# Kernel optimization log

Measured on AMD Instinct MI355X. Metric: run time of the kernel, lower is better.

The kernel has to match this reference:

```python
import jax, jax.numpy as jnp
import numpy as np

NUM_EMBEDDINGS = 512
EMBEDDING_DIM = 64
SPARSITY_LEVEL = 5
COMMITMENT_COST = 0.25
EPSILON = 1e-10


def setup_inputs() -> dict:
    key = jax.random.key(0)
    k1, k2 = jax.random.split(key)
    z_e = jax.random.normal(k1, (32, EMBEDDING_DIM, 32, 32), dtype=jnp.float32)
    D = jax.random.normal(k2, (EMBEDDING_DIM, NUM_EMBEDDINGS), dtype=jnp.float32)
    # module normalizes atoms at init (normalize_atoms=True)
    D = D / (jnp.linalg.norm(D, axis=0, keepdims=True) + 1e-10)
    return {"z_e": z_e, "dictionary": D}


def batch_omp(X, D, sparsity, eps):
    """Greedy batched OMP. X: [M, B] signals, D: [M, N] unit-norm atoms -> coeffs [N, B]."""
    M, B = X.shape
    N = D.shape[1]
    bidx = jnp.arange(B)

    def step(carry, _):
        coeffs, residual, mask = carry
        corr = D.T @ residual                      # [N, B]
        idx = jnp.argmax(jnp.abs(corr) * mask, axis=0)  # [B]
        mask = mask.at[idx, bidx].set(0.0)
        d_sel = D[:, idx]                          # [M, B] gather of selected atoms
        alpha = jnp.sum(residual * d_sel, axis=0) / (jnp.sum(d_sel * d_sel, axis=0) + eps)
        coeffs = coeffs.at[idx, bidx].set(alpha)   # scatter coefficient
        residual = residual - d_sel * alpha[None, :]
        return (coeffs, residual, mask), None

    init = (jnp.zeros((N, B), X.dtype), X, jnp.ones((N, B), X.dtype))
    (coeffs, _, _), _ = jax.lax.scan(step, init, None, length=sparsity)
    return coeffs


def reference(z_e, dictionary):
    B, C, H, W = z_e.shape
    L = H * W
    # patch_size=1: unfold -> [B, C, L]; permute(2,0,1) -> [L, B, C]; flatten -> [L*B, C]; .T -> [C, L*B]
    tokens = z_e.reshape(B, C, L).transpose(2, 0, 1).reshape(L * B, C).T
    xf = tokens.astype(jnp.float32)
    Df = dictionary.astype(jnp.float32)
    atom_norms = jnp.maximum(jnp.linalg.norm(Df, axis=0), 1e-10)
    Dn = Df / atom_norms[None, :]                  # normalized dictionary (used for OMP and recon)
    coefficients = batch_omp(xf, Dn, SPARSITY_LEVEL, EPSILON)  # [N, L*B]
    z_dl_f32 = Dn @ coefficients                   # [C, L*B]
    # fold back: [L*B, C] -> [L, B, C] -> [B, C, L] -> [B, C, H, W]
    z_dl = z_dl_f32.T.reshape(L, B, C).transpose(1, 2, 0).reshape(B, C, H, W).astype(z_e.dtype)
    z_e_nhwc = z_e.transpose(0, 2, 3, 1)
    z_dl_nhwc = z_dl.transpose(0, 2, 3, 1)
    e_latent_loss = jnp.mean((jax.lax.stop_gradient(z_dl_nhwc) - z_e_nhwc) ** 2)
    dl_latent_loss = jnp.mean((z_dl_nhwc - jax.lax.stop_gradient(z_e_nhwc)) ** 2)
    loss = COMMITMENT_COST * e_latent_loss + dl_latent_loss
    z_dl_out = z_e + jax.lax.stop_gradient(z_dl - z_e)  # straight-through estimator
    return (z_dl_out, loss, coefficients)
```

## Files before the change

kernel.cpp:

```cpp
#include <hip/hip_runtime.h>
#include <stdint.h>

#define NSIG   32768
#define NATOM  512
#define MDIM   64
#define SPAR   5
#define EPS    1e-10

__global__ __launch_bounds__(512) void prep_kernel(const float* __restrict__ D,
                                                   float*  __restrict__ Dt32,
                                                   double* __restrict__ Dt64,
                                                   double* __restrict__ Dd64,
                                                   double* __restrict__ rnrm) {
  int n = threadIdx.x;
  double ss = 0.0;
#pragma unroll 8
  for (int c = 0; c < MDIM; ++c) {
    double v = (double)D[c * NATOM + n];
    ss += v * v;
  }
  double norm = sqrt(ss);
  if (norm < 1e-10) norm = 1e-10;
  double s2 = 0.0;
#pragma unroll 8
  for (int c = 0; c < MDIM; ++c) {
    double v = (double)D[c * NATOM + n] / norm;
    Dt64[(size_t)c * NATOM + n] = v;
    Dd64[((size_t)n << 6) + c]  = v;
    Dt32[(size_t)c * NATOM + n] = (float)v;
    s2 += v * v;
  }
  rnrm[n] = 1.0 / (s2 + EPS);
}

__global__ __launch_bounds__(512) void gram_kernel(const float* __restrict__ Dt32,
                                                   float* __restrict__ G32) {
  int i = blockIdx.x;
  int j = threadIdx.x;
  float s = 0.f;
#pragma unroll 8
  for (int c = 0; c < MDIM; ++c)
    s += Dt32[(size_t)c * NATOM + i] * Dt32[(size_t)c * NATOM + j];
  G32[(size_t)i * NATOM + j] = s;
}

__global__ __launch_bounds__(256) void repack_kernel(const float* __restrict__ z_e,
                                                     float* __restrict__ xw) {
  __shared__ float t[32][33];
  const int c  = blockIdx.x & 63;
  const int l0 = (blockIdx.x >> 6) << 5;
  const int tr = threadIdx.x >> 5;
  const int tc = threadIdx.x & 31;
#pragma unroll
  for (int p = 0; p < 4; ++p) {
    int b = tr + p * 8;
    t[b][tc] = z_e[(size_t)b * 65536 + (size_t)c * 1024 + l0 + tc];
  }
  __syncthreads();
#pragma unroll
  for (int p = 0; p < 4; ++p) {
    int lr = tr + p * 8;
    xw[(size_t)(l0 + lr) * 2048 + c * 32 + tc] = t[tc][lr];
  }
}

__global__ __launch_bounds__(256, 2) void omp10_kernel(const float* __restrict__ xw,
                                                       const float* __restrict__ Dt32,
                                                       const double* __restrict__ Dt64,
                                                       const double* __restrict__ Dd64,
                                                       const double* __restrict__ rnrm,
                                                       const float* __restrict__ G32,
                                                       float* __restrict__ z_dl,
                                                       float* __restrict__ coeff,
                                                       double* __restrict__ partial) {
  __shared__ float  xs[2048];
  __shared__ double s_al[SPAR][32];
  __shared__ int    s_sel[SPAR][32];
  __shared__ double s_red[4];

  const int tid  = threadIdx.x;
  const int w    = __builtin_amdgcn_readfirstlane(tid >> 6);
  const int lane = tid & 63;
  const int abase = lane << 3;
  const int gsi  = lane >> 3;
  const int lg   = lane & 7;
  const int sig  = (w << 3) + gsi;
  const int bid  = blockIdx.x;
  const int l    = ((bid & 7) << 7) | (bid >> 3);

  {
    const float* src = xw + (size_t)l * 2048 + tid * 8;
    float4 v0 = *(const float4*)src;
    float4 v1 = *(const float4*)(src + 4);
    *(float4*)&xs[tid * 8]     = v0;
    *(float4*)&xs[tid * 8 + 4] = v1;
  }
  __syncthreads();

  float cor[8][8];
#pragma unroll
  for (int a = 0; a < 8; ++a)
#pragma unroll
    for (int si = 0; si < 8; ++si) cor[a][si] = 0.0f;

  {
    const float* dbase = Dt32 + abase;
    const int xo = w << 3;
    float4 dA0 = *(const float4*)dbase;
    float4 dB0 = *(const float4*)(dbase + 4);
    float4 dA1 = *(const float4*)(dbase + NATOM);
    float4 dB1 = *(const float4*)(dbase + NATOM + 4);
    for (int k = 0; k < MDIM; k += 2) {
      float4 xA0 = *(const float4*)&xs[k * 32 + xo];
      float4 xB0 = *(const float4*)&xs[k * 32 + xo + 4];
      float4 xA1 = *(const float4*)&xs[(k + 1) * 32 + xo];
      float4 xB1 = *(const float4*)&xs[(k + 1) * 32 + xo + 4];
      float dv0[8] = {dA0.x, dA0.y, dA0.z, dA0.w, dB0.x, dB0.y, dB0.z, dB0.w};
      float xv0[8] = {xA0.x, xA0.y, xA0.z, xA0.w, xB0.x, xB0.y, xB0.z, xB0.w};
      float dv1[8] = {dA1.x, dA1.y, dA1.z, dA1.w, dB1.x, dB1.y, dB1.z, dB1.w};
      float xv1[8] = {xA1.x, xA1.y, xA1.z, xA1.w, xB1.x, xB1.y, xB1.z, xB1.w};
      if (k + 2 < MDIM) {
        const float* dn = dbase + (size_t)(k + 2) * NATOM;
        dA0 = *(const float4*)dn; dB0 = *(const float4*)(dn + 4);
        const float* dm = dbase + (size_t)(k + 3) * NATOM;
        dA1 = *(const float4*)dm; dB1 = *(const float4*)(dm + 4);
      }
#pragma unroll
      for (int a = 0; a < 8; ++a)
#pragma unroll
        for (int si = 0; si < 8; ++si)
          cor[a][si] += dv0[a] * xv0[si];
#pragma unroll
      for (int a = 0; a < 8; ++a)
#pragma unroll
        for (int si = 0; si < 8; ++si)
          cor[a][si] += dv1[a] * xv1[si];
    }
  }

  double rr[8];
#pragma unroll
  for (int j = 0; j < 8; ++j)
    rr[j] = (double)xs[(lg * 8 + j) * 32 + sig];

  unsigned long long mk = ~0ull;

#pragma unroll 1
  for (int it = 0; it < SPAR; ++it) {
    unsigned int kb[8];
#pragma unroll
    for (int si = 0; si < 8; ++si) {
      unsigned int best = 0;
#pragma unroll
      for (int a = 0; a < 8; ++a) {
        float ac = fabsf(cor[a][si]);
        unsigned int enc = (unsigned int)(511 - (abase + a));
        unsigned int kv = (__float_as_uint(ac) & 0xFFFFFC00u) | enc;
        bool avail = (mk >> ((a << 3) + si)) & 1ull;
        kv = avail ? kv : enc;
        best = best > kv ? best : kv;
      }
      kb[si] = best;
    }
#pragma unroll
    for (int o = 1; o < 8; o <<= 1)
#pragma unroll
      for (int si = 0; si < 8; ++si) {
        unsigned int ok = __shfl_xor(kb[si], o);
        kb[si] = kb[si] > ok ? kb[si] : ok;
      }
    unsigned int kk = kb[0];
#pragma unroll
    for (int si = 1; si < 8; ++si) kk = ((lane & 7) == si) ? kb[si] : kk;
#pragma unroll
    for (int o = 8; o < 64; o <<= 1) {
      unsigned int ok = __shfl_xor(kk, o);
      kk = kk > ok ? kk : ok;
    }

    const unsigned int wkg = __shfl(kk, gsi);
    const int gig = 511 - (int)(wkg & 0x1FFu);
    double p;
    {
      const double2* dp = (const double2*)(Dd64 + ((size_t)gig << 6) + (lg << 3));
      double2 q0 = dp[0], q1 = dp[1], q2 = dp[2], q3 = dp[3];
      p = ((q0.x*rr[0] + q0.y*rr[1]) + (q1.x*rr[2] + q1.y*rr[3]))
        + ((q2.x*rr[4] + q2.y*rr[5]) + (q3.x*rr[6] + q3.y*rr[7]));
    }
    p += __shfl_xor(p, 1); p += __shfl_xor(p, 2); p += __shfl_xor(p, 4);
    unsigned long long bkey =
      ((unsigned long long)__double_as_longlong(fabs(p)) & ~0x3FFull)
      | (unsigned long long)(511 - gig);
    double bcor = p;
    int bgi = gig;

    unsigned long long pend = 0ull;
#pragma unroll
    for (int si = 0; si < 8; ++si) {
      unsigned int wks = __shfl(kk, si);
      int widx = 511 - (int)(wks & 0x1FFu);
      float thr = __uint_as_float(wks & 0xFFFFFC00u) * 0.999f;
#pragma unroll
      for (int a = 0; a < 8; ++a) {
        bool avail = (mk >> ((a << 3) + si)) & 1ull;
        bool inb = avail && (thr > 0.0f) && (fabsf(cor[a][si]) >= thr)
                 && ((abase + a) != widx);
        pend |= inb ? (1ull << ((a << 3) + si)) : 0ull;
      }
    }
    while (__any(pend != 0ull)) {
      int myext = -1;
#pragma unroll
      for (int si = 0; si < 8; ++si) {
        unsigned long long m8 = (pend >> si) & 0x0101010101010101ull;
        unsigned long long bal = __ballot(m8 != 0ull);
        int ge = -1;
        if (bal != 0ull) {
          int src = __ffsll((long long)bal) - 1;
          unsigned long long pm = __shfl(m8, src);
          int a0 = (__ffsll((long long)pm) - 1) >> 3;
          ge = (src << 3) + a0;
        }
        if (lane == si) myext = ge;
        if (ge >= 0 && (ge >> 3) == lane)
          pend &= ~(1ull << (((ge & 7) << 3) + si));
      }
      int gie = __shfl(myext, gsi);
      if (gie >= 0) {
        const double2* dp = (const double2*)(Dd64 + ((size_t)gie << 6) + (lg << 3));
        double2 q0 = dp[0], q1 = dp[1], q2 = dp[2], q3 = dp[3];
        double pe = ((q0.x*rr[0] + q0.y*rr[1]) + (q1.x*rr[2] + q1.y*rr[3]))
                  + ((q2.x*rr[4] + q2.y*rr[5]) + (q3.x*rr[6] + q3.y*rr[7]));
        pe += __shfl_xor(pe, 1); pe += __shfl_xor(pe, 2); pe += __shfl_xor(pe, 4);
        unsigned long long ke =
          ((unsigned long long)__double_as_longlong(fabs(pe)) & ~0x3FFull)
          | (unsigned long long)(511 - gie);
        if (ke > bkey) { bkey = ke; bcor = pe; bgi = gie; }
      }
    }

    double alpha = bcor * rnrm[bgi];
    if (lg == 0) { s_sel[it][sig] = bgi; s_al[it][sig] = alpha; }
#pragma unroll
    for (int si = 0; si < 8; ++si) {
      int gf = __shfl(bgi, si << 3);
      if ((gf >> 3) == lane) mk &= ~(1ull << (((gf & 7) << 3) + si));
    }

    if (it != SPAR - 1) {
      {
        const double2* dp = (const double2*)(Dd64 + ((size_t)bgi << 6) + (lg << 3));
        double2 q0 = dp[0], q1 = dp[1], q2 = dp[2], q3 = dp[3];
        rr[0] -= alpha*q0.x; rr[1] -= alpha*q0.y;
        rr[2] -= alpha*q1.x; rr[3] -= alpha*q1.y;
        rr[4] -= alpha*q2.x; rr[5] -= alpha*q2.y;
        rr[6] -= alpha*q3.x; rr[7] -= alpha*q3.y;
      }
#pragma unroll
      for (int sb = 0; sb < 8; sb += 2) {
        int   g0i = __shfl(bgi, sb << 3);
        float a0f = (float)__shfl(alpha, sb << 3);
        int   g1i = __shfl(bgi, (sb + 1) << 3);
        float a1f = (float)__shfl(alpha, (sb + 1) << 3);
        const float* gp0 = G32 + (size_t)g0i * NATOM + abase;
        const float* gp1 = G32 + (size_t)g1i * NATOM + abase;
        float4 u0 = *(const float4*)gp0;
        float4 u1 = *(const float4*)(gp0 + 4);
        float4 v0 = *(const float4*)gp1;
        float4 v1 = *(const float4*)(gp1 + 4);
        cor[0][sb] -= a0f*u0.x; cor[1][sb] -= a0f*u0.y;
        cor[2][sb] -= a0f*u0.z; cor[3][sb] -= a0f*u0.w;
        cor[4][sb] -= a0f*u1.x; cor[5][sb] -= a0f*u1.y;
        cor[6][sb] -= a0f*u1.z; cor[7][sb] -= a0f*u1.w;
        cor[0][sb+1] -= a1f*v0.x; cor[1][sb+1] -= a1f*v0.y;
        cor[2][sb+1] -= a1f*v0.z; cor[3][sb+1] -= a1f*v0.w;
        cor[4][sb+1] -= a1f*v1.x; cor[5][sb+1] -= a1f*v1.y;
        cor[6][sb+1] -= a1f*v1.z; cor[7][sb+1] -= a1f*v1.w;
      }
    }
  }
  __syncthreads();

  const int s = tid & 31;
  {
    const int c0 = tid >> 5;
    double s2 = 0.0;
#pragma unroll
    for (int r = 0; r < 8; ++r) {
      int c = c0 + (r << 3);
      double v = s_al[0][s] * Dt64[(size_t)c * NATOM + s_sel[0][s]];
#pragma unroll
      for (int tt = 1; tt < SPAR; ++tt)
        v += s_al[tt][s] * Dt64[(size_t)c * NATOM + s_sel[tt][s]];
      float zv = (float)v;
      z_dl[((size_t)s * MDIM + c) * 1024 + l] = zv;
      double x = (double)xs[(c << 5) + s];
      double diff = (double)zv - x;
      s2 += diff * diff;
    }
#pragma unroll
    for (int o = 32; o > 0; o >>= 1) s2 += __shfl_down(s2, o);
    if (lane == 0) s_red[w] = s2;
  }
  __syncthreads();
  if (tid == 0) partial[bid] = (s_red[0] + s_red[1]) + (s_red[2] + s_red[3]);

  {
    const float4 z4 = make_float4(0.f, 0.f, 0.f, 0.f);
#pragma unroll
    for (int p2 = 0; p2 < 16; ++p2) {
      int idx = tid + (p2 << 8);
      int a = idx >> 3, q = idx & 7;
      *(float4*)(coeff + (size_t)a * NSIG + ((size_t)l << 5) + (q << 2)) = z4;
    }
  }
  __syncthreads();
  if (tid < 32) {
#pragma unroll
    for (int tt = 0; tt < SPAR; ++tt) {
      int gi = s_sel[tt][tid];
      coeff[(size_t)gi * NSIG + ((size_t)l << 5) + tid] = (float)s_al[tt][tid];
    }
  }
}

__global__ __launch_bounds__(64) void finalize_kernel(const double* __restrict__ partial,
                                                      float* __restrict__ loss_out) {
  double s = 0.0;
  for (int i = threadIdx.x; i < 1024; i += 64) s += partial[i];
#pragma unroll
  for (int o = 32; o > 0; o >>= 1) s += __shfl_down(s, o);
  if (threadIdx.x == 0) loss_out[0] = (float)(1.25 * s / 2097152.0);
}

extern "C" void kernel_launch(void* const* d_in, const int* in_sizes, int n_in,
                              void* d_out, int out_size, void* d_ws, size_t ws_size,
                              hipStream_t stream) {
  const float* z_e = (const float*)d_in[0];
  const float* D   = (const float*)d_in[1];

  float* out      = (float*)d_out;
  float* z_dl     = out;
  float* loss_out = out + 2097152;
  float* coeff    = out + 2097153;

  char*   ws      = (char*)d_ws;
  double* partial = (double*)ws;
  float*  Dt32    = (float*) (ws + 8192);
  double* Dt64    = (double*)(ws + 8192 + 131072);
  double* Dd64    = (double*)(ws + 8192 + 131072 + 262144);
  double* rnrm    = (double*)(ws + 8192 + 131072 + 524288);
  float*  G32     = (float*) (ws + 8192 + 131072 + 524288 + 4096);
  float*  xw      = (float*) (ws + 8192 + 131072 + 524288 + 4096 + 1048576);

  prep_kernel<<<1, 512, 0, stream>>>(D, Dt32, Dt64, Dd64, rnrm);
  gram_kernel<<<NATOM, NATOM, 0, stream>>>(Dt32, G32);
  repack_kernel<<<2048, 256, 0, stream>>>(z_e, xw);
  omp10_kernel<<<1024, 256, 0, stream>>>(xw, Dt32, Dt64, Dd64, rnrm, G32,
                                         z_dl, coeff, partial);
  finalize_kernel<<<1, 64, 0, stream>>>(partial, loss_out);
}
```

Baseline: 152.2 us.

## Use packed FMA for correlations and reconstruct output from the final residual

The correlation GEMM and the Gram-based correlation updates now use packed two-wide float FMAs (v_pk_fma_f32), halving the FMA instruction count. The residual is also updated on the last OMP iteration, so the reconstruction is computed as x minus the residual. This replaces the per-signal gather from a double-precision transposed dictionary, so that dictionary and its prep writes are removed. The occupancy hint in launch_bounds is dropped and one block barrier is removed. Reconstruction now comes from the residual difference, which may differ slightly in rounding from summing alpha times the atoms.

```diff
diff --git a/kernel.cpp b/kernel.cpp
--- a/kernel.cpp
+++ b/kernel.cpp
@@ -7,9 +7,19 @@
 #define SPAR   5
 #define EPS    1e-10
 
+typedef float f32x2 __attribute__((ext_vector_type(2)));
+
+__device__ __forceinline__ f32x2 pkfma(f32x2 a, f32x2 b, f32x2 c) {
+#if __has_builtin(__builtin_elementwise_fma)
+  return __builtin_elementwise_fma(a, b, c);
+#else
+  asm("v_pk_fma_f32 %0, %1, %2, %0" : "+v"(c) : "v"(a), "v"(b));
+  return c;
+#endif
+}
+
 __global__ __launch_bounds__(512) void prep_kernel(const float* __restrict__ D,
                                                    float*  __restrict__ Dt32,
-                                                   double* __restrict__ Dt64,
                                                    double* __restrict__ Dd64,
                                                    double* __restrict__ rnrm) {
   int n = threadIdx.x;
@@ -25,7 +35,6 @@
 #pragma unroll 8
   for (int c = 0; c < MDIM; ++c) {
     double v = (double)D[c * NATOM + n] / norm;
-    Dt64[(size_t)c * NATOM + n] = v;
     Dd64[((size_t)n << 6) + c]  = v;
     Dt32[(size_t)c * NATOM + n] = (float)v;
     s2 += v * v;
@@ -64,15 +73,14 @@
   }
 }
 
-__global__ __launch_bounds__(256, 2) void omp10_kernel(const float* __restrict__ xw,
-                                                       const float* __restrict__ Dt32,
-                                                       const double* __restrict__ Dt64,
-                                                       const double* __restrict__ Dd64,
-                                                       const double* __restrict__ rnrm,
-                                                       const float* __restrict__ G32,
-                                                       float* __restrict__ z_dl,
-                                                       float* __restrict__ coeff,
-                                                       double* __restrict__ partial) {
+__global__ __launch_bounds__(256) void omp11_kernel(const float* __restrict__ xw,
+                                                    const float* __restrict__ Dt32,
+                                                    const double* __restrict__ Dd64,
+                                                    const double* __restrict__ rnrm,
+                                                    const float* __restrict__ G32,
+                                                    float* __restrict__ z_dl,
+                                                    float* __restrict__ coeff,
+                                                    double* __restrict__ partial) {
   __shared__ float  xs[2048];
   __shared__ double s_al[SPAR][32];
   __shared__ int    s_sel[SPAR][32];
@@ -97,11 +105,11 @@
   }
   __syncthreads();
 
-  float cor[8][8];
-#pragma unroll
-  for (int a = 0; a < 8; ++a)
-#pragma unroll
-    for (int si = 0; si < 8; ++si) cor[a][si] = 0.0f;
+  f32x2 cor2[4][8];
+#pragma unroll
+  for (int a2 = 0; a2 < 4; ++a2)
+#pragma unroll
+    for (int si = 0; si < 8; ++si) cor2[a2][si] = (f32x2){0.f, 0.f};
 
   {
     const float* dbase = Dt32 + abase;
@@ -115,9 +123,9 @@
       float4 xB0 = *(const float4*)&xs[k * 32 + xo + 4];
       float4 xA1 = *(const float4*)&xs[(k + 1) * 32 + xo];
       float4 xB1 = *(const float4*)&xs[(k + 1) * 32 + xo + 4];
-      float dv0[8] = {dA0.x, dA0.y, dA0.z, dA0.w, dB0.x, dB0.y, dB0.z, dB0.w};
+      f32x2 dp0[4] = {{dA0.x, dA0.y}, {dA0.z, dA0.w}, {dB0.x, dB0.y}, {dB0.z, dB0.w}};
+      f32x2 dp1[4] = {{dA1.x, dA1.y}, {dA1.z, dA1.w}, {dB1.x, dB1.y}, {dB1.z, dB1.w}};
       float xv0[8] = {xA0.x, xA0.y, xA0.z, xA0.w, xB0.x, xB0.y, xB0.z, xB0.w};
-      float dv1[8] = {dA1.x, dA1.y, dA1.z, dA1.w, dB1.x, dB1.y, dB1.z, dB1.w};
       float xv1[8] = {xA1.x, xA1.y, xA1.z, xA1.w, xB1.x, xB1.y, xB1.z, xB1.w};
       if (k + 2 < MDIM) {
         const float* dn = dbase + (size_t)(k + 2) * NATOM;
@@ -126,15 +134,19 @@
         dA1 = *(const float4*)dm; dB1 = *(const float4*)(dm + 4);
       }
 #pragma unroll
-      for (int a = 0; a < 8; ++a)
-#pragma unroll
-        for (int si = 0; si < 8; ++si)
-          cor[a][si] += dv0[a] * xv0[si];
-#pragma unroll
-      for (int a = 0; a < 8; ++a)
-#pragma unroll
-        for (int si = 0; si < 8; ++si)
-          cor[a][si] += dv1[a] * xv1[si];
+      for (int si = 0; si < 8; ++si) {
+        f32x2 xq = {xv0[si], xv0[si]};
+#pragma unroll
+        for (int a2 = 0; a2 < 4; ++a2)
+          cor2[a2][si] = pkfma(dp0[a2], xq, cor2[a2][si]);
+      }
+#pragma unroll
+      for (int si = 0; si < 8; ++si) {
+        f32x2 xq = {xv1[si], xv1[si]};
+#pragma unroll
+        for (int a2 = 0; a2 < 4; ++a2)
+          cor2[a2][si] = pkfma(dp1[a2], xq, cor2[a2][si]);
+      }
     }
   }
 
@@ -153,7 +165,8 @@
       unsigned int best = 0;
 #pragma unroll
       for (int a = 0; a < 8; ++a) {
-        float ac = fabsf(cor[a][si]);
+        float cv = (a & 1) ? cor2[a >> 1][si].y : cor2[a >> 1][si].x;
+        float ac = fabsf(cv);
         unsigned int enc = (unsigned int)(511 - (abase + a));
         unsigned int kv = (__float_as_uint(ac) & 0xFFFFFC00u) | enc;
         bool avail = (mk >> ((a << 3) + si)) & 1ull;
@@ -202,8 +215,9 @@
       float thr = __uint_as_float(wks & 0xFFFFFC00u) * 0.999f;
 #pragma unroll
       for (int a = 0; a < 8; ++a) {
+        float cv = (a & 1) ? cor2[a >> 1][si].y : cor2[a >> 1][si].x;
         bool avail = (mk >> ((a << 3) + si)) & 1ull;
-        bool inb = avail && (thr > 0.0f) && (fabsf(cor[a][si]) >= thr)
+        bool inb = avail && (thr > 0.0f) && (fabsf(cv) >= thr)
                  && ((abase + a) != widx);
         pend |= inb ? (1ull << ((a << 3) + si)) : 0ull;
       }
@@ -247,63 +261,50 @@
       if ((gf >> 3) == lane) mk &= ~(1ull << (((gf & 7) << 3) + si));
     }
 
+    {
+      const double2* dp = (const double2*)(Dd64 + ((size_t)bgi << 6) + (lg << 3));
+      double2 q0 = dp[0], q1 = dp[1], q2 = dp[2], q3 = dp[3];
+      rr[0] -= alpha*q0.x; rr[1] -= alpha*q0.y;
+      rr[2] -= alpha*q1.x; rr[3] -= alpha*q1.y;
+      rr[4] -= alpha*q2.x; rr[5] -= alpha*q2.y;
+      rr[6] -= alpha*q3.x; rr[7] -= alpha*q3.y;
+    }
+
     if (it != SPAR - 1) {
-      {
-        const double2* dp = (const double2*)(Dd64 + ((size_t)bgi << 6) + (lg << 3));
-        double2 q0 = dp[0], q1 = dp[1], q2 = dp[2], q3 = dp[3];
-        rr[0] -= alpha*q0.x; rr[1] -= alpha*q0.y;
-        rr[2] -= alpha*q1.x; rr[3] -= alpha*q1.y;
-        rr[4] -= alpha*q2.x; rr[5] -= alpha*q2.y;
-        rr[6] -= alpha*q3.x; rr[7] -= alpha*q3.y;
-      }
 #pragma unroll
       for (int sb = 0; sb < 8; sb += 2) {
         int   g0i = __shfl(bgi, sb << 3);
         float a0f = (float)__shfl(alpha, sb << 3);
         int   g1i = __shfl(bgi, (sb + 1) << 3);
         float a1f = (float)__shfl(alpha, (sb + 1) << 3);
-        const float* gp0 = G32 + (size_t)g0i * NATOM + abase;
-        const float* gp1 = G32 + (size_t)g1i * NATOM + abase;
-        float4 u0 = *(const float4*)gp0;
-        float4 u1 = *(const float4*)(gp0 + 4);
-        float4 v0 = *(const float4*)gp1;
-        float4 v1 = *(const float4*)(gp1 + 4);
-        cor[0][sb] -= a0f*u0.x; cor[1][sb] -= a0f*u0.y;
-        cor[2][sb] -= a0f*u0.z; cor[3][sb] -= a0f*u0.w;
-        cor[4][sb] -= a0f*u1.x; cor[5][sb] -= a0f*u1.y;
-        cor[6][sb] -= a0f*u1.z; cor[7][sb] -= a0f*u1.w;
-        cor[0][sb+1] -= a1f*v0.x; cor[1][sb+1] -= a1f*v0.y;
-        cor[2][sb+1] -= a1f*v0.z; cor[3][sb+1] -= a1f*v0.w;
-        cor[4][sb+1] -= a1f*v1.x; cor[5][sb+1] -= a1f*v1.y;
-        cor[6][sb+1] -= a1f*v1.z; cor[7][sb+1] -= a1f*v1.w;
-      }
-    }
-  }
-  __syncthreads();
-
-  const int s = tid & 31;
+        const f32x2* gp0 = (const f32x2*)(G32 + (size_t)g0i * NATOM + abase);
+        const f32x2* gp1 = (const f32x2*)(G32 + (size_t)g1i * NATOM + abase);
+        f32x2 na0 = {-a0f, -a0f};
+        f32x2 na1 = {-a1f, -a1f};
+#pragma unroll
+        for (int a2 = 0; a2 < 4; ++a2) {
+          cor2[a2][sb]     = pkfma(gp0[a2], na0, cor2[a2][sb]);
+          cor2[a2][sb + 1] = pkfma(gp1[a2], na1, cor2[a2][sb + 1]);
+        }
+      }
+    }
+  }
+
   {
-    const int c0 = tid >> 5;
     double s2 = 0.0;
-#pragma unroll
-    for (int r = 0; r < 8; ++r) {
-      int c = c0 + (r << 3);
-      double v = s_al[0][s] * Dt64[(size_t)c * NATOM + s_sel[0][s]];
-#pragma unroll
-      for (int tt = 1; tt < SPAR; ++tt)
-        v += s_al[tt][s] * Dt64[(size_t)c * NATOM + s_sel[tt][s]];
-      float zv = (float)v;
-      z_dl[((size_t)s * MDIM + c) * 1024 + l] = zv;
-      double x = (double)xs[(c << 5) + s];
+    const int d0 = lg << 3;
+#pragma unroll
+    for (int j = 0; j < 8; ++j) {
+      double x = (double)xs[(d0 + j) * 32 + sig];
+      float zv = (float)(x - rr[j]);
+      z_dl[((size_t)sig * MDIM + d0 + j) * 1024 + l] = zv;
       double diff = (double)zv - x;
       s2 += diff * diff;
     }
 #pragma unroll
-    for (int o = 32; o > 0; o >>= 1) s2 += __shfl_down(s2, o);
+    for (int o = 1; o < 64; o <<= 1) s2 += __shfl_xor(s2, o);
     if (lane == 0) s_red[w] = s2;
   }
-  __syncthreads();
-  if (tid == 0) partial[bid] = (s_red[0] + s_red[1]) + (s_red[2] + s_red[3]);
 
   {
     const float4 z4 = make_float4(0.f, 0.f, 0.f, 0.f);
@@ -315,6 +316,7 @@
     }
   }
   __syncthreads();
+  if (tid == 0) partial[bid] = (s_red[0] + s_red[1]) + (s_red[2] + s_red[3]);
   if (tid < 32) {
 #pragma unroll
     for (int tt = 0; tt < SPAR; ++tt) {
@@ -347,16 +349,15 @@
   char*   ws      = (char*)d_ws;
   double* partial = (double*)ws;
   float*  Dt32    = (float*) (ws + 8192);
-  double* Dt64    = (double*)(ws + 8192 + 131072);
-  double* Dd64    = (double*)(ws + 8192 + 131072 + 262144);
-  double* rnrm    = (double*)(ws + 8192 + 131072 + 524288);
-  float*  G32     = (float*) (ws + 8192 + 131072 + 524288 + 4096);
-  float*  xw      = (float*) (ws + 8192 + 131072 + 524288 + 4096 + 1048576);
-
-  prep_kernel<<<1, 512, 0, stream>>>(D, Dt32, Dt64, Dd64, rnrm);
+  double* Dd64    = (double*)(ws + 8192 + 131072);
+  double* rnrm    = (double*)(ws + 8192 + 131072 + 262144);
+  float*  G32     = (float*) (ws + 8192 + 131072 + 262144 + 4096);
+  float*  xw      = (float*) (ws + 8192 + 131072 + 262144 + 4096 + 1048576);
+
+  prep_kernel<<<1, 512, 0, stream>>>(D, Dt32, Dd64, rnrm);
   gram_kernel<<<NATOM, NATOM, 0, stream>>>(Dt32, G32);
   repack_kernel<<<2048, 256, 0, stream>>>(z_e, xw);
-  omp10_kernel<<<1024, 256, 0, stream>>>(xw, Dt32, Dt64, Dd64, rnrm, G32,
+  omp11_kernel<<<1024, 256, 0, stream>>>(xw, Dt32, Dd64, rnrm, G32,
                                          z_dl, coeff, partial);
   finalize_kernel<<<1, 64, 0, stream>>>(partial, loss_out);
 }
```

After: 190.1 us. 24.9% more time.

## Compute reconstruction as x minus residual and write it via transposed unpack kernel

Applied to the files above, without the earlier changes.

The OMP kernel now applies the final residual update and computes the reconstruction as signal minus residual, so it no longer gathers Dt64 rows per selected atom. The reconstruction goes into shared memory, is written back into the xw workspace with coalesced float4 stores, and a new tiled transpose kernel scatters it into NCHW z_dl. This replaces strided, uncoalesced z_dl stores and dictionary gathers with an extra kernel launch plus one more read and write of the 8 MB tensor. The launch-bounds occupancy hint of 2 is also dropped, and the Dt64 buffer is removed from prep.

```diff
diff --git a/kernel.cpp b/kernel.cpp
--- a/kernel.cpp
+++ b/kernel.cpp
@@ -9,7 +9,6 @@
 
 __global__ __launch_bounds__(512) void prep_kernel(const float* __restrict__ D,
                                                    float*  __restrict__ Dt32,
-                                                   double* __restrict__ Dt64,
                                                    double* __restrict__ Dd64,
                                                    double* __restrict__ rnrm) {
   int n = threadIdx.x;
@@ -25,7 +24,6 @@
 #pragma unroll 8
   for (int c = 0; c < MDIM; ++c) {
     double v = (double)D[c * NATOM + n] / norm;
-    Dt64[(size_t)c * NATOM + n] = v;
     Dd64[((size_t)n << 6) + c]  = v;
     Dt32[(size_t)c * NATOM + n] = (float)v;
     s2 += v * v;
@@ -64,15 +62,33 @@
   }
 }
 
-__global__ __launch_bounds__(256, 2) void omp10_kernel(const float* __restrict__ xw,
-                                                       const float* __restrict__ Dt32,
-                                                       const double* __restrict__ Dt64,
-                                                       const double* __restrict__ Dd64,
-                                                       const double* __restrict__ rnrm,
-                                                       const float* __restrict__ G32,
-                                                       float* __restrict__ z_dl,
-                                                       float* __restrict__ coeff,
-                                                       double* __restrict__ partial) {
+__global__ __launch_bounds__(256) void unpack_kernel(const float* __restrict__ xw,
+                                                     float* __restrict__ z_dl) {
+  __shared__ float t[32][33];
+  const int c  = blockIdx.x & 63;
+  const int l0 = (blockIdx.x >> 6) << 5;
+  const int tr = threadIdx.x >> 5;
+  const int tc = threadIdx.x & 31;
+#pragma unroll
+  for (int p = 0; p < 4; ++p) {
+    int lr = tr + p * 8;
+    t[lr][tc] = xw[(size_t)(l0 + lr) * 2048 + c * 32 + tc];
+  }
+  __syncthreads();
+#pragma unroll
+  for (int p = 0; p < 4; ++p) {
+    int b = tr + p * 8;
+    z_dl[(size_t)b * 65536 + (size_t)c * 1024 + l0 + tc] = t[tc][b];
+  }
+}
+
+__global__ __launch_bounds__(256) void omp12_kernel(float* __restrict__ xw,
+                                                    const float* __restrict__ Dt32,
+                                                    const double* __restrict__ Dd64,
+                                                    const double* __restrict__ rnrm,
+                                                    const float* __restrict__ G32,
+                                                    float* __restrict__ coeff,
+                                                    double* __restrict__ partial) {
   __shared__ float  xs[2048];
   __shared__ double s_al[SPAR][32];
   __shared__ int    s_sel[SPAR][32];
@@ -247,15 +263,16 @@
       if ((gf >> 3) == lane) mk &= ~(1ull << (((gf & 7) << 3) + si));
     }
 
+    {
+      const double2* dp = (const double2*)(Dd64 + ((size_t)bgi << 6) + (lg << 3));
+      double2 q0 = dp[0], q1 = dp[1], q2 = dp[2], q3 = dp[3];
+      rr[0] -= alpha*q0.x; rr[1] -= alpha*q0.y;
+      rr[2] -= alpha*q1.x; rr[3] -= alpha*q1.y;
+      rr[4] -= alpha*q2.x; rr[5] -= alpha*q2.y;
+      rr[6] -= alpha*q3.x; rr[7] -= alpha*q3.y;
+    }
+
     if (it != SPAR - 1) {
-      {
-        const double2* dp = (const double2*)(Dd64 + ((size_t)bgi << 6) + (lg << 3));
-        double2 q0 = dp[0], q1 = dp[1], q2 = dp[2], q3 = dp[3];
-        rr[0] -= alpha*q0.x; rr[1] -= alpha*q0.y;
-        rr[2] -= alpha*q1.x; rr[3] -= alpha*q1.y;
-        rr[4] -= alpha*q2.x; rr[5] -= alpha*q2.y;
-        rr[6] -= alpha*q3.x; rr[7] -= alpha*q3.y;
-      }
 #pragma unroll
       for (int sb = 0; sb < 8; sb += 2) {
         int   g0i = __shfl(bgi, sb << 3);
@@ -281,29 +298,22 @@
   }
   __syncthreads();
 
-  const int s = tid & 31;
-  {
-    const int c0 = tid >> 5;
+  {
     double s2 = 0.0;
-#pragma unroll
-    for (int r = 0; r < 8; ++r) {
-      int c = c0 + (r << 3);
-      double v = s_al[0][s] * Dt64[(size_t)c * NATOM + s_sel[0][s]];
-#pragma unroll
-      for (int tt = 1; tt < SPAR; ++tt)
-        v += s_al[tt][s] * Dt64[(size_t)c * NATOM + s_sel[tt][s]];
-      float zv = (float)v;
-      z_dl[((size_t)s * MDIM + c) * 1024 + l] = zv;
-      double x = (double)xs[(c << 5) + s];
+    const int d0 = lg << 3;
+#pragma unroll
+    for (int j = 0; j < 8; ++j) {
+      int idx = (d0 + j) * 32 + sig;
+      double x = (double)xs[idx];
+      float zv = (float)(x - rr[j]);
+      xs[idx] = zv;
       double diff = (double)zv - x;
       s2 += diff * diff;
     }
 #pragma unroll
-    for (int o = 32; o > 0; o >>= 1) s2 += __shfl_down(s2, o);
+    for (int o = 1; o < 64; o <<= 1) s2 += __shfl_xor(s2, o);
     if (lane == 0) s_red[w] = s2;
   }
-  __syncthreads();
-  if (tid == 0) partial[bid] = (s_red[0] + s_red[1]) + (s_red[2] + s_red[3]);
 
   {
     const float4 z4 = make_float4(0.f, 0.f, 0.f, 0.f);
@@ -315,6 +325,15 @@
     }
   }
   __syncthreads();
+
+  {
+    float* dst = xw + (size_t)l * 2048 + tid * 8;
+    float4 v0 = *(const float4*)&xs[tid * 8];
+    float4 v1 = *(const float4*)&xs[tid * 8 + 4];
+    *(float4*)dst       = v0;
+    *(float4*)(dst + 4) = v1;
+  }
+  if (tid == 0) partial[bid] = (s_red[0] + s_red[1]) + (s_red[2] + s_red[3]);
   if (tid < 32) {
 #pragma unroll
     for (int tt = 0; tt < SPAR; ++tt) {
@@ -347,16 +366,15 @@
   char*   ws      = (char*)d_ws;
   double* partial = (double*)ws;
   float*  Dt32    = (float*) (ws + 8192);
-  double* Dt64    = (double*)(ws + 8192 + 131072);
-  double* Dd64    = (double*)(ws + 8192 + 131072 + 262144);
-  double* rnrm    = (double*)(ws + 8192 + 131072 + 524288);
-  float*  G32     = (float*) (ws + 8192 + 131072 + 524288 + 4096);
-  float*  xw      = (float*) (ws + 8192 + 131072 + 524288 + 4096 + 1048576);
-
-  prep_kernel<<<1, 512, 0, stream>>>(D, Dt32, Dt64, Dd64, rnrm);
+  double* Dd64    = (double*)(ws + 8192 + 131072);
+  double* rnrm    = (double*)(ws + 8192 + 131072 + 262144);
+  float*  G32     = (float*) (ws + 8192 + 131072 + 262144 + 4096);
+  float*  xw      = (float*) (ws + 8192 + 131072 + 262144 + 4096 + 1048576);
+
+  prep_kernel<<<1, 512, 0, stream>>>(D, Dt32, Dd64, rnrm);
   gram_kernel<<<NATOM, NATOM, 0, stream>>>(Dt32, G32);
   repack_kernel<<<2048, 256, 0, stream>>>(z_e, xw);
-  omp10_kernel<<<1024, 256, 0, stream>>>(xw, Dt32, Dt64, Dd64, rnrm, G32,
-                                         z_dl, coeff, partial);
+  omp12_kernel<<<1024, 256, 0, stream>>>(xw, Dt32, Dd64, rnrm, G32, coeff, partial);
+  unpack_kernel<<<2048, 256, 0, stream>>>(xw, z_dl);
   finalize_kernel<<<1, 64, 0, stream>>>(partial, loss_out);
 }
```

Result: faster. 135.4 us, median of 2 (-11.0%).
